# Performance work log

Measured on AMD Instinct MI355X. Metric: run time of the kernel, lower is better.

Reference implementation:

```python
import jax, jax.numpy as jnp
import numpy as np

B, T, H, N, D, L, V = 4, 1024, 4, 4096, 256, 6, 256
Dh = N // H  # per-head dim; RoPE max_pos == Dh so T <= Dh
EPS = 1e-5


def _ln(x):
    # LayerNorm over last dim, no affine, eps=1e-5 (torch default)
    m = jnp.mean(x, axis=-1, keepdims=True)
    v = jnp.mean((x - m) ** 2, axis=-1, keepdims=True)
    return (x - m) / jnp.sqrt(v + EPS)


def _rope_tables(seq_len, head_dim):
    inv_freq = 1.0 / (10000.0 ** (jnp.arange(0, head_dim, 2, dtype=jnp.float32) / head_dim))
    t = jnp.arange(seq_len, dtype=jnp.float32)
    freqs = jnp.outer(t, inv_freq)            # [T, Dh/2]
    emb = jnp.concatenate([freqs, freqs], -1)  # [T, Dh]
    return jnp.cos(emb), jnp.sin(emb)


def _rotate_half(x):
    d = x.shape[-1]
    return jnp.concatenate([-x[..., d // 2:], x[..., :d // 2]], axis=-1)


def setup_inputs() -> dict:
    key = jax.random.key(0)
    ks = jax.random.split(key, 6)
    tokens = jax.random.randint(ks[0], (B, T), 0, V)
    emb_w = 0.02 * jax.random.normal(ks[1], (V, D), dtype=jnp.float32)
    E = 0.02 * jax.random.normal(ks[2], (N, D), dtype=jnp.float32)
    Dx = 0.02 * jax.random.normal(ks[3], (H, D, Dh), dtype=jnp.float32)
    Dy = 0.02 * jax.random.normal(ks[4], (H, D, Dh), dtype=jnp.float32)
    readout = 0.02 * jax.random.normal(ks[5], (D, V), dtype=jnp.float32)
    return {"tokens": tokens, "emb_w": emb_w, "E": E, "Dx": Dx, "Dy": Dy, "readout": readout}


def reference(tokens, emb_w, E, Dx, Dy, readout):
    b, t = tokens.shape
    dh = Dx.shape[-1]
    cos, sin = _rope_tables(t, dh)  # [T, Dh], broadcast over B,H
    v = _ln(emb_w[tokens])          # [B, T, D]
    for _ in range(L):
        x = jax.nn.relu(jnp.einsum('btd,hde->bhte', v, Dx))       # [B,H,T,Dh]
        xr = x * cos + _rotate_half(x) * sin                       # RoPE (Q and K share)
        scores = jnp.einsum('bhte,bhse->bhts', xr, xr)             # [B,H,T,T] (no softmax)
        a = jnp.einsum('bhts,bsd->bhtd', scores, v)                # [B,H,T,D]
        y = jax.nn.relu(jnp.einsum('bhtd,hde->bhte', a, Dy)) * x   # [B,H,T,Dh]
        y = jnp.transpose(y, (0, 2, 1, 3)).reshape(b, t, -1)       # [B,T,N]
        v = _ln(v + _ln(y @ E))
    return v @ readout  # [B,T,V]
```

## Files before the change

### kernel.cpp

```cpp
#include <hip/hip_runtime.h>
#include <cstdint>

namespace {

typedef _Float16 f16_t;
typedef _Float16 f16x8 __attribute__((ext_vector_type(8)));
typedef _Float16 f16x4 __attribute__((ext_vector_type(4)));
typedef float    f32x4 __attribute__((ext_vector_type(4)));

constexpr int Bc = 4, Tc = 1024, Hc = 4, Dc = 256, DHc = 1024, Lc = 6, Vc = 256;
constexpr int HALFc = 512;
constexpr float EPS = 1e-5f;
constexpr long long T4q  = (long long)Tc * 4096;
constexpr long long TDq  = (long long)Tc * Dc;
constexpr long long DTq  = (long long)Dc * Tc;
constexpr long long HDDq = (long long)DHc * Dc;
constexpr long long TBUFq = (long long)Bc * Tc * Dc;

__device__ __forceinline__ int pe_perm(int v) {
  return (v & ~1023) | ((v & 511) << 1) | ((v >> 9) & 1);
}

__device__ __forceinline__ void gload16(const void* g, void* l) {
  __builtin_amdgcn_global_load_lds((const __attribute__((address_space(1))) void*)g,
                                   (__attribute__((address_space(3))) void*)l, 16, 0, 0);
}

template<int EPI, bool BKMAJ, int NW>
__global__ __launch_bounds__(NW * 64)
void gemm_f16(const f16_t* __restrict__ A, long long sAb, long long sAh,
              const f16_t* __restrict__ B, long long sBb, long long sBh,
              void* __restrict__ Cv, long long sCb, long long sCh,
              const f16_t* __restrict__ aux,
              int K, int lda, int ldb, int ldc,
              const float* __restrict__ cosP, const float* __restrict__ sinP)
{
  constexpr int FN   = (NW == 4) ? 4 : 2;
  constexpr int NTHR = NW * 64;
  constexpr int SP   = 1024 / NTHR;
  constexpr int RPP  = NTHR / 8;

  __shared__ __align__(16) f16_t As[128 * 64];
  __shared__ __align__(16) f16_t Bs[128 * 64];

  const int zb = blockIdx.z >> 2, zh = blockIdx.z & 3;
  A += zb * sAb + zh * sAh;
  B += zb * sBb + zh * sBh;
  const long long Coff = zb * sCb + zh * sCh;

  const int tid  = threadIdx.x;
  const int lane = tid & 63;
  const int wave = tid >> 6;
  const int wr = (NW == 4) ? (wave >> 1) : (wave >> 2);
  const int wc = (NW == 4) ? (wave & 1)  : (wave & 3);
  const int m0 = blockIdx.y * 128, n0 = blockIdx.x * 128;

  const int lrow  = tid >> 3;
  const int lslot = tid & 7;
  const int kp = tid & 31, g = tid >> 5;

  f32x4 acc[4][FN] = {};

  for (int k0 = 0; k0 < K; k0 += 64) {
    #pragma unroll
    for (int c = 0; c < SP; ++c) {
      const int row  = c * RPP + lrow;
      const int scol = (lslot ^ (row & 7)) << 3;
      gload16(A + (size_t)(m0 + row) * lda + k0 + scol, &As[(c * NTHR + tid) * 8]);
    }
    if (!BKMAJ) {
      #pragma unroll
      for (int c = 0; c < SP; ++c) {
        const int row  = c * RPP + lrow;
        const int scol = (lslot ^ (row & 7)) << 3;
        gload16(B + (size_t)(n0 + row) * ldb + k0 + scol, &Bs[(c * NTHR + tid) * 8]);
      }
    } else {
      constexpr int NP = (NW == 4) ? 2 : 1;
      const int k = kp * 2;
      #pragma unroll
      for (int p = 0; p < NP; ++p) {
        const int nb = p * 64 + g * 8;
        const f16x8 r0 = *(const f16x8*)(B + (size_t)(k0 + k) * ldb + n0 + nb);
        const f16x8 r1 = *(const f16x8*)(B + (size_t)(k0 + k + 1) * ldb + n0 + nb);
        #pragma unroll
        for (int j = 0; j < 8; ++j) {
          const int n = nb + j;
          union { f16_t h[2]; unsigned int u; } pk;
          pk.h[0] = r0[j]; pk.h[1] = r1[j];
          ((unsigned int*)Bs)[n * 32 + (((kp >> 2) ^ (n & 7)) << 2) + (kp & 3)] = pk.u;
        }
      }
    }
    __syncthreads();

    #pragma unroll
    for (int ks = 0; ks < 2; ++ks) {
      f16x8 af[4], bf[FN];
      #pragma unroll
      for (int m = 0; m < 4; ++m) {
        const int r  = wr * 64 + m * 16 + (lane & 15);
        const int sl = (ks * 4 + (lane >> 4)) ^ (r & 7);
        af[m] = *(const f16x8*)(&As[r * 64 + sl * 8]);
      }
      #pragma unroll
      for (int n = 0; n < FN; ++n) {
        const int r  = wc * (FN * 16) + n * 16 + (lane & 15);
        const int sl = (ks * 4 + (lane >> 4)) ^ (r & 7);
        bf[n] = *(const f16x8*)(&Bs[r * 64 + sl * 8]);
      }
      #pragma unroll
      for (int m = 0; m < 4; ++m)
        #pragma unroll
        for (int n = 0; n < FN; ++n)
          acc[m][n] = __builtin_amdgcn_mfma_f32_16x16x32_f16(af[m], bf[n], acc[m][n], 0, 0, 0);
    }
    __syncthreads();
  }

  const int cr   = (lane >> 4) * 4;
  const int ccol = lane & 15;
  if (EPI == 4) {
    float* C = (float*)Cv + Coff;
    #pragma unroll
    for (int m = 0; m < 4; ++m)
      #pragma unroll
      for (int n = 0; n < FN; ++n)
        #pragma unroll
        for (int r = 0; r < 4; ++r)
          C[(long long)(m0 + wr * 64 + m * 16 + cr + r) * ldc
            + (n0 + wc * (FN * 16) + n * 16 + ccol)] = acc[m][n][r];
  } else if (EPI == 5) {
    f16_t* X  = (f16_t*)Cv;
    f16_t* XR = const_cast<f16_t*>(aux);
    #pragma unroll
    for (int m = 0; m < 4; ++m)
      #pragma unroll
      for (int n = 0; n < FN; ++n) {
        const int gcol = n0 + wc * (FN * 16) + n * 16 + ccol;
        const int jj   = (gcol & 1023) >> 1;
        const float sg = (gcol & 1) ? 1.0f : -1.0f;
        #pragma unroll
        for (int r = 0; r < 4; ++r) {
          const int grow = m0 + wr * 64 + m * 16 + cr + r;
          const int tt   = grow & (Tc - 1);
          const float val  = fmaxf(acc[m][n][r], 0.0f);
          const float part = __shfl_xor(val, 1);
          const float c = cosP[tt * HALFc + jj];
          const float s = sinP[tt * HALFc + jj];
          const float xrv = val * c + part * s * sg;
          const long long off = (long long)grow * ldc + gcol;
          X[off]  = (f16_t)val;
          XR[off] = (f16_t)xrv;
        }
      }
  } else {
    f16_t* C = (f16_t*)Cv + Coff;
    const f16_t* X = (EPI == 2) ? aux + Coff : nullptr;
    #pragma unroll
    for (int m = 0; m < 4; ++m)
      #pragma unroll
      for (int n = 0; n < FN; ++n)
        #pragma unroll
        for (int r = 0; r < 4; ++r) {
          const long long off = (long long)(m0 + wr * 64 + m * 16 + cr + r) * ldc
                                + (n0 + wc * (FN * 16) + n * 16 + ccol);
          float val = acc[m][n][r];
          if (EPI >= 1) val = fmaxf(val, 0.0f);
          if (EPI == 2) val *= (float)X[off];
          C[off] = (f16_t)val;
        }
  }
}

__global__ __launch_bounds__(256)
void transpose_f32_f16(const float* __restrict__ in, f16_t* __restrict__ out,
                       int R, int C, long long sIn, long long sOut,
                       int permR, int permC)
{
  __shared__ float tile[32][33];
  in  += (long long)blockIdx.z * sIn;
  out += (long long)blockIdx.z * sOut;
  const int c0 = blockIdx.x * 32, r0 = blockIdx.y * 32;
  const int tx = threadIdx.x & 31, ty = threadIdx.x >> 5;
  #pragma unroll
  for (int i = 0; i < 32; i += 8)
    tile[ty + i][tx] = in[(long long)(r0 + ty + i) * C + (c0 + tx)];
  __syncthreads();
  #pragma unroll
  for (int i = 0; i < 32; i += 8) {
    int ro = c0 + ty + i;
    int co = r0 + tx;
    if (permR) ro = pe_perm(ro);
    if (permC) co = pe_perm(co);
    out[(long long)ro * R + co] = (f16_t)tile[tx][ty + i];
  }
}

__global__ __launch_bounds__(256)
void transpose_f16(const f16_t* __restrict__ in, f16_t* __restrict__ out,
                   int R, int C, long long sIn, long long sOut)
{
  __shared__ f16_t tile[32][34];
  in  += (long long)blockIdx.z * sIn;
  out += (long long)blockIdx.z * sOut;
  const int c0 = blockIdx.x * 32, r0 = blockIdx.y * 32;
  const int tx = threadIdx.x & 31, ty = threadIdx.x >> 5;
  #pragma unroll
  for (int i = 0; i < 32; i += 8)
    tile[ty + i][tx] = in[(long long)(r0 + ty + i) * C + (c0 + tx)];
  __syncthreads();
  #pragma unroll
  for (int i = 0; i < 32; i += 8)
    out[(long long)(c0 + ty + i) * R + (r0 + tx)] = tile[tx][ty + i];
}

__global__ __launch_bounds__(256)
void init_tables(float* __restrict__ cosT, float* __restrict__ sinT)
{
  const int i = blockIdx.x * 256 + threadIdx.x;
  const int j = i & (HALFc - 1);
  const int t = i >> 9;
  const float inv = expf(-(float)j * (9.210340371976184f / 512.0f));
  const float ang = (float)t * inv;
  cosT[i] = cosf(ang);
  sinT[i] = sinf(ang);
}

__device__ __forceinline__ void block_stats(float val, float* red, float& mean, float& inv_std)
{
  float s1 = val, s2 = val * val;
  #pragma unroll
  for (int o = 1; o < 64; o <<= 1) {
    s1 += __shfl_xor(s1, o);
    s2 += __shfl_xor(s2, o);
  }
  const int lane = threadIdx.x & 63;
  const int w = threadIdx.x >> 6;
  if (lane == 0) { red[w * 2] = s1; red[w * 2 + 1] = s2; }
  __syncthreads();
  s1 = red[0] + red[2] + red[4] + red[6];
  s2 = red[1] + red[3] + red[5] + red[7];
  mean = s1 * (1.0f / Dc);
  const float var = s2 * (1.0f / Dc) - mean * mean;
  inv_std = 1.0f / sqrtf(var + EPS);
  __syncthreads();
}

__global__ __launch_bounds__(256)
void embed_ln(const int* __restrict__ tokens, const float* __restrict__ emb,
              f16_t* __restrict__ v)
{
  __shared__ float red[8];
  const int row = blockIdx.x;
  const int d = threadIdx.x;
  const float val = emb[(long long)tokens[row] * Dc + d];
  float m, is;
  block_stats(val, red, m, is);
  v[(long long)row * Dc + d] = (f16_t)((val - m) * is);
}

__global__ __launch_bounds__(256)
void fuse_ln4(f16_t* __restrict__ v, const float* __restrict__ t)
{
  __shared__ float red[8];
  const long long row = blockIdx.x;
  const int d = threadIdx.x;
  const long long off = row * Dc + d;
  const float tv = t[off] + t[off + TBUFq] + t[off + 2 * TBUFq] + t[off + 3 * TBUFq];
  float m1, is1;
  block_stats(tv, red, m1, is1);
  const float u = (tv - m1) * is1;
  const float wv = (float)v[off] + u;
  float m2, is2;
  block_stats(wv, red, m2, is2);
  v[off] = (f16_t)((wv - m2) * is2);
}

}

extern "C" void kernel_launch(void* const* d_in, const int* in_sizes, int n_in,
                              void* d_out, int out_size, void* d_ws, size_t ws_size,
                              hipStream_t stream)
{
  (void)in_sizes; (void)n_in; (void)out_size; (void)ws_size;
  const int*   tokens  = (const int*)d_in[0];
  const float* emb_w   = (const float*)d_in[1];
  const float* E       = (const float*)d_in[2];
  const float* Dx      = (const float*)d_in[3];
  const float* Dy      = (const float*)d_in[4];
  const float* readout = (const float*)d_in[5];
  float* out = (float*)d_out;

  char* w = (char*)d_ws;
  auto carve = [&](size_t bytes) { char* p = w; w += (bytes + 255) & ~(size_t)255; return p; };
  float* cosT = (float*)carve((size_t)Tc * HALFc * 4);
  float* sinT = (float*)carve((size_t)Tc * HALFc * 4);
  f16_t* v    = (f16_t*)carve((size_t)Bc * Tc * Dc * 2);
  f16_t* vT   = (f16_t*)carve((size_t)Bc * Dc * Tc * 2);
  f16_t* x    = (f16_t*)carve((size_t)Bc * Tc * 4096 * 2);
  f16_t* xr   = (f16_t*)carve((size_t)Bc * Tc * 4096 * 2);
  f16_t* WT   = (f16_t*)carve((size_t)Bc * Dc * 4096 * 2);
  f16_t* a    = (f16_t*)carve((size_t)Bc * Tc * Hc * Dc * 2);
  float* t    = (float*)carve((size_t)4 * TBUFq * 4);
  f16_t* DxT  = (f16_t*)carve((size_t)Hc * DHc * Dc * 2);
  f16_t* DyT  = (f16_t*)carve((size_t)Hc * DHc * Dc * 2);
  f16_t* ET   = (f16_t*)carve((size_t)Dc * Hc * DHc * 2);
  f16_t* RT   = (f16_t*)carve((size_t)Vc * Dc * 2);

  transpose_f32_f16<<<dim3(32, 8, Hc), 256, 0, stream>>>(Dx, DxT, Dc, DHc, HDDq, HDDq, 1, 0);
  transpose_f32_f16<<<dim3(32, 8, Hc), 256, 0, stream>>>(Dy, DyT, Dc, DHc, HDDq, HDDq, 1, 0);
  transpose_f32_f16<<<dim3(8, 128, 1), 256, 0, stream>>>(E, ET, 4096, Dc, 0, 0, 0, 1);
  transpose_f32_f16<<<dim3(8, 8, 1), 256, 0, stream>>>(readout, RT, Dc, Vc, 0, 0, 0, 0);
  init_tables<<<(Tc * HALFc) / 256, 256, 0, stream>>>(cosT, sinT);
  embed_ln<<<Bc * Tc, 256, 0, stream>>>(tokens, emb_w, v);
  transpose_f16<<<dim3(8, 32, Bc), 256, 0, stream>>>(v, vT, Tc, Dc, TDq, DTq);

  for (int l = 0; l < Lc; ++l) {
    gemm_f16<5, false, 4><<<dim3(32, 32, 1), 256, 0, stream>>>(
        v, 0, 0, DxT, 0, 0, x, 0, 0, xr, Dc, Dc, Dc, 4096, cosT, sinT);
    gemm_f16<0, true, 8><<<dim3(32, 2, 4), 512, 0, stream>>>(
        vT, 0, DTq, xr, 0, T4q, WT, 0, (long long)Dc * 4096, nullptr,
        Tc, Tc, 4096, 4096, nullptr, nullptr);
    gemm_f16<0, false, 8><<<dim3(2, 8, 16), 512, 0, stream>>>(
        xr, T4q, DHc, WT, (long long)Dc * 4096, DHc, a, (long long)Tc * 1024, Dc,
        nullptr, DHc, 4096, 4096, 1024, nullptr, nullptr);
    gemm_f16<2, false, 4><<<dim3(8, 32, 4), 256, 0, stream>>>(
        a, 0, Dc, DyT, 0, HDDq, xr, 0, DHc, x, Dc, 1024, Dc, 4096, nullptr, nullptr);
    gemm_f16<4, false, 8><<<dim3(2, 32, 4), 512, 0, stream>>>(
        xr, 0, DHc, ET, 0, DHc, t, 0, TBUFq, nullptr, DHc, 4096, 4096, Dc,
        nullptr, nullptr);
    fuse_ln4<<<Bc * Tc, 256, 0, stream>>>(v, t);
    transpose_f16<<<dim3(8, 32, Bc), 256, 0, stream>>>(v, vT, Tc, Dc, TDq, DTq);
  }

  gemm_f16<4, false, 8><<<dim3(2, 32, 1), 512, 0, stream>>>(
      v, 0, 0, RT, 0, 0, out, 0, 0, nullptr, Dc, Dc, Dc, Vc, nullptr, nullptr);
}
```

Baseline: 810.6 us.

## Drop separate x buffer and vT transpose; recover x from xr via inverse RoPE

The first GEMM now writes only the RoPE-rotated xr, and the Dy GEMM epilogue recovers x by applying the inverse rotation to xr (which it overwrites) before multiplying. The per-layer f16 transpose of v is removed; the k-major staging path now also reads A directly from v. This removes a large f16 write and read of x plus a transpose kernel per layer. In exchange, x is rebuilt from an f16-rounded xr, which adds rounding error, and the k-major A staging uses non-async register loads instead of direct-to-LDS loads.

```diff
diff --git a/kernel.cpp b/kernel.cpp
--- a/kernel.cpp
+++ b/kernel.cpp
@@ -5,7 +5,6 @@
 
 typedef _Float16 f16_t;
 typedef _Float16 f16x8 __attribute__((ext_vector_type(8)));
-typedef _Float16 f16x4 __attribute__((ext_vector_type(4)));
 typedef float    f32x4 __attribute__((ext_vector_type(4)));
 
 constexpr int Bc = 4, Tc = 1024, Hc = 4, Dc = 256, DHc = 1024, Lc = 6, Vc = 256;
@@ -13,7 +12,6 @@
 constexpr float EPS = 1e-5f;
 constexpr long long T4q  = (long long)Tc * 4096;
 constexpr long long TDq  = (long long)Tc * Dc;
-constexpr long long DTq  = (long long)Dc * Tc;
 constexpr long long HDDq = (long long)DHc * Dc;
 constexpr long long TBUFq = (long long)Bc * Tc * Dc;
 
@@ -26,12 +24,32 @@
                                    (__attribute__((address_space(3))) void*)l, 16, 0, 0);
 }
 
-template<int EPI, bool BKMAJ, int NW>
+template<int NW>
+__device__ __forceinline__ void stage_kmaj(const f16_t* __restrict__ P, int k0,
+                                           int ld, int c0, f16_t* S,
+                                           int kp, int g) {
+  constexpr int NP = (NW == 4) ? 2 : 1;
+  const int k = kp * 2;
+  #pragma unroll
+  for (int p = 0; p < NP; ++p) {
+    const int nb = p * 64 + g * 8;
+    const f16x8 r0 = *(const f16x8*)(P + (size_t)(k0 + k) * ld + c0 + nb);
+    const f16x8 r1 = *(const f16x8*)(P + (size_t)(k0 + k + 1) * ld + c0 + nb);
+    #pragma unroll
+    for (int j = 0; j < 8; ++j) {
+      const int n = nb + j;
+      union { f16_t h[2]; unsigned int u; } pk;
+      pk.h[0] = r0[j]; pk.h[1] = r1[j];
+      ((unsigned int*)S)[n * 32 + (((kp >> 2) ^ (n & 7)) << 2) + (kp & 3)] = pk.u;
+    }
+  }
+}
+
+template<int EPI, bool AKMAJ, bool BKMAJ, int NW>
 __global__ __launch_bounds__(NW * 64)
 void gemm_f16(const f16_t* __restrict__ A, long long sAb, long long sAh,
               const f16_t* __restrict__ B, long long sBb, long long sBh,
               void* __restrict__ Cv, long long sCb, long long sCh,
-              const f16_t* __restrict__ aux,
               int K, int lda, int ldb, int ldc,
               const float* __restrict__ cosP, const float* __restrict__ sinP)
 {
@@ -62,11 +80,15 @@
   f32x4 acc[4][FN] = {};
 
   for (int k0 = 0; k0 < K; k0 += 64) {
-    #pragma unroll
-    for (int c = 0; c < SP; ++c) {
-      const int row  = c * RPP + lrow;
-      const int scol = (lslot ^ (row & 7)) << 3;
-      gload16(A + (size_t)(m0 + row) * lda + k0 + scol, &As[(c * NTHR + tid) * 8]);
+    if (!AKMAJ) {
+      #pragma unroll
+      for (int c = 0; c < SP; ++c) {
+        const int row  = c * RPP + lrow;
+        const int scol = (lslot ^ (row & 7)) << 3;
+        gload16(A + (size_t)(m0 + row) * lda + k0 + scol, &As[(c * NTHR + tid) * 8]);
+      }
+    } else {
+      stage_kmaj<NW>(A, k0, lda, m0, As, kp, g);
     }
     if (!BKMAJ) {
       #pragma unroll
@@ -76,21 +98,7 @@
         gload16(B + (size_t)(n0 + row) * ldb + k0 + scol, &Bs[(c * NTHR + tid) * 8]);
       }
     } else {
-      constexpr int NP = (NW == 4) ? 2 : 1;
-      const int k = kp * 2;
-      #pragma unroll
-      for (int p = 0; p < NP; ++p) {
-        const int nb = p * 64 + g * 8;
-        const f16x8 r0 = *(const f16x8*)(B + (size_t)(k0 + k) * ldb + n0 + nb);
-        const f16x8 r1 = *(const f16x8*)(B + (size_t)(k0 + k + 1) * ldb + n0 + nb);
-        #pragma unroll
-        for (int j = 0; j < 8; ++j) {
-          const int n = nb + j;
-          union { f16_t h[2]; unsigned int u; } pk;
-          pk.h[0] = r0[j]; pk.h[1] = r1[j];
-          ((unsigned int*)Bs)[n * 32 + (((kp >> 2) ^ (n & 7)) << 2) + (kp & 3)] = pk.u;
-        }
-      }
+      stage_kmaj<NW>(B, k0, ldb, n0, Bs, kp, g);
     }
     __syncthreads();
 
@@ -131,8 +139,7 @@
           C[(long long)(m0 + wr * 64 + m * 16 + cr + r) * ldc
             + (n0 + wc * (FN * 16) + n * 16 + ccol)] = acc[m][n][r];
   } else if (EPI == 5) {
-    f16_t* X  = (f16_t*)Cv;
-    f16_t* XR = const_cast<f16_t*>(aux);
+    f16_t* C = (f16_t*)Cv + Coff;
     #pragma unroll
     for (int m = 0; m < 4; ++m)
       #pragma unroll
@@ -148,28 +155,41 @@
           const float part = __shfl_xor(val, 1);
           const float c = cosP[tt * HALFc + jj];
           const float s = sinP[tt * HALFc + jj];
-          const float xrv = val * c + part * s * sg;
+          C[(long long)grow * ldc + gcol] = (f16_t)(val * c + part * s * sg);
+        }
+      }
+  } else if (EPI == 2) {
+    f16_t* C = (f16_t*)Cv + Coff;
+    #pragma unroll
+    for (int m = 0; m < 4; ++m)
+      #pragma unroll
+      for (int n = 0; n < FN; ++n) {
+        const int gcol = n0 + wc * (FN * 16) + n * 16 + ccol;
+        const int jj   = (gcol & 1023) >> 1;
+        const float sg = (gcol & 1) ? 1.0f : -1.0f;
+        #pragma unroll
+        for (int r = 0; r < 4; ++r) {
+          const int grow = m0 + wr * 64 + m * 16 + cr + r;
+          const int tt   = grow & (Tc - 1);
           const long long off = (long long)grow * ldc + gcol;
-          X[off]  = (f16_t)val;
-          XR[off] = (f16_t)xrv;
+          const float xrv  = (float)C[off];
+          const float part = __shfl_xor(xrv, 1);
+          const float c = cosP[tt * HALFc + jj];
+          const float s = sinP[tt * HALFc + jj];
+          const float xv = xrv * c - part * s * sg;
+          C[off] = (f16_t)(fmaxf(acc[m][n][r], 0.0f) * xv);
         }
       }
   } else {
     f16_t* C = (f16_t*)Cv + Coff;
-    const f16_t* X = (EPI == 2) ? aux + Coff : nullptr;
     #pragma unroll
     for (int m = 0; m < 4; ++m)
       #pragma unroll
       for (int n = 0; n < FN; ++n)
         #pragma unroll
-        for (int r = 0; r < 4; ++r) {
-          const long long off = (long long)(m0 + wr * 64 + m * 16 + cr + r) * ldc
-                                + (n0 + wc * (FN * 16) + n * 16 + ccol);
-          float val = acc[m][n][r];
-          if (EPI >= 1) val = fmaxf(val, 0.0f);
-          if (EPI == 2) val *= (float)X[off];
-          C[off] = (f16_t)val;
-        }
+        for (int r = 0; r < 4; ++r)
+          C[(long long)(m0 + wr * 64 + m * 16 + cr + r) * ldc
+            + (n0 + wc * (FN * 16) + n * 16 + ccol)] = (f16_t)acc[m][n][r];
   }
 }
 
@@ -198,24 +218,6 @@
 }
 
 __global__ __launch_bounds__(256)
-void transpose_f16(const f16_t* __restrict__ in, f16_t* __restrict__ out,
-                   int R, int C, long long sIn, long long sOut)
-{
-  __shared__ f16_t tile[32][34];
-  in  += (long long)blockIdx.z * sIn;
-  out += (long long)blockIdx.z * sOut;
-  const int c0 = blockIdx.x * 32, r0 = blockIdx.y * 32;
-  const int tx = threadIdx.x & 31, ty = threadIdx.x >> 5;
-  #pragma unroll
-  for (int i = 0; i < 32; i += 8)
-    tile[ty + i][tx] = in[(long long)(r0 + ty + i) * C + (c0 + tx)];
-  __syncthreads();
-  #pragma unroll
-  for (int i = 0; i < 32; i += 8)
-    out[(long long)(c0 + ty + i) * R + (r0 + tx)] = tile[tx][ty + i];
-}
-
-__global__ __launch_bounds__(256)
 void init_tables(float* __restrict__ cosT, float* __restrict__ sinT)
 {
   const int i = blockIdx.x * 256 + threadIdx.x;
@@ -297,8 +299,6 @@
   float* cosT = (float*)carve((size_t)Tc * HALFc * 4);
   float* sinT = (float*)carve((size_t)Tc * HALFc * 4);
   f16_t* v    = (f16_t*)carve((size_t)Bc * Tc * Dc * 2);
-  f16_t* vT   = (f16_t*)carve((size_t)Bc * Dc * Tc * 2);
-  f16_t* x    = (f16_t*)carve((size_t)Bc * Tc * 4096 * 2);
   f16_t* xr   = (f16_t*)carve((size_t)Bc * Tc * 4096 * 2);
   f16_t* WT   = (f16_t*)carve((size_t)Bc * Dc * 4096 * 2);
   f16_t* a    = (f16_t*)carve((size_t)Bc * Tc * Hc * Dc * 2);
@@ -314,26 +314,24 @@
   transpose_f32_f16<<<dim3(8, 8, 1), 256, 0, stream>>>(readout, RT, Dc, Vc, 0, 0, 0, 0);
   init_tables<<<(Tc * HALFc) / 256, 256, 0, stream>>>(cosT, sinT);
   embed_ln<<<Bc * Tc, 256, 0, stream>>>(tokens, emb_w, v);
-  transpose_f16<<<dim3(8, 32, Bc), 256, 0, stream>>>(v, vT, Tc, Dc, TDq, DTq);
 
   for (int l = 0; l < Lc; ++l) {
-    gemm_f16<5, false, 4><<<dim3(32, 32, 1), 256, 0, stream>>>(
-        v, 0, 0, DxT, 0, 0, x, 0, 0, xr, Dc, Dc, Dc, 4096, cosT, sinT);
-    gemm_f16<0, true, 8><<<dim3(32, 2, 4), 512, 0, stream>>>(
-        vT, 0, DTq, xr, 0, T4q, WT, 0, (long long)Dc * 4096, nullptr,
-        Tc, Tc, 4096, 4096, nullptr, nullptr);
-    gemm_f16<0, false, 8><<<dim3(2, 8, 16), 512, 0, stream>>>(
+    gemm_f16<5, false, false, 4><<<dim3(32, 32, 1), 256, 0, stream>>>(
+        v, 0, 0, DxT, 0, 0, xr, 0, 0, Dc, Dc, Dc, 4096, cosT, sinT);
+    gemm_f16<0, true, true, 8><<<dim3(32, 2, 4), 512, 0, stream>>>(
+        v, 0, TDq, xr, 0, T4q, WT, 0, (long long)Dc * 4096,
+        Tc, Dc, 4096, 4096, nullptr, nullptr);
+    gemm_f16<0, false, false, 8><<<dim3(2, 8, 16), 512, 0, stream>>>(
         xr, T4q, DHc, WT, (long long)Dc * 4096, DHc, a, (long long)Tc * 1024, Dc,
-        nullptr, DHc, 4096, 4096, 1024, nullptr, nullptr);
-    gemm_f16<2, false, 4><<<dim3(8, 32, 4), 256, 0, stream>>>(
-        a, 0, Dc, DyT, 0, HDDq, xr, 0, DHc, x, Dc, 1024, Dc, 4096, nullptr, nullptr);
-    gemm_f16<4, false, 8><<<dim3(2, 32, 4), 512, 0, stream>>>(
-        xr, 0, DHc, ET, 0, DHc, t, 0, TBUFq, nullptr, DHc, 4096, 4096, Dc,
+        DHc, 4096, 4096, 1024, nullptr, nullptr);
+    gemm_f16<2, false, false, 4><<<dim3(8, 32, 4), 256, 0, stream>>>(
+        a, 0, Dc, DyT, 0, HDDq, xr, 0, DHc, Dc, 1024, Dc, 4096, cosT, sinT);
+    gemm_f16<4, false, false, 8><<<dim3(2, 32, 4), 512, 0, stream>>>(
+        xr, 0, DHc, ET, 0, DHc, t, 0, TBUFq, DHc, 4096, 4096, Dc,
         nullptr, nullptr);
     fuse_ln4<<<Bc * Tc, 256, 0, stream>>>(v, t);
-    transpose_f16<<<dim3(8, 32, Bc), 256, 0, stream>>>(v, vT, Tc, Dc, TDq, DTq);
-  }
-
-  gemm_f16<4, false, 8><<<dim3(2, 32, 1), 512, 0, stream>>>(
-      v, 0, 0, RT, 0, 0, out, 0, 0, nullptr, Dc, Dc, Dc, Vc, nullptr, nullptr);
-}
+  }
+
+  gemm_f16<4, false, false, 8><<<dim3(2, 32, 1), 512, 0, stream>>>(
+      v, 0, 0, RT, 0, 0, out, 0, 0, Dc, Dc, Dc, Vc, nullptr, nullptr);
+}
```

Result: slower. 953.2 us (+17.6%).
